# Performance work log

Measured on AMD Instinct MI355X. Metric: run time of the kernel, lower is better.

Reference implementation:

```python
import jax, jax.numpy as jnp
import numpy as np

B, F, H, L, K = 16384, 1024, 1024, 256, 7

def _lin(key, fi, fo, lead=()):
    k1, k2 = jax.random.split(key)
    s = 1.0 / np.sqrt(fi)
    W = jax.random.uniform(k1, lead + (fi, fo), jnp.float32, -s, s)
    b = jax.random.uniform(k2, lead + (fo,), jnp.float32, -s, s)
    return W, b

def setup_inputs() -> dict:
    ks = jax.random.split(jax.random.key(0), 16)
    x = jax.random.normal(ks[0], (B, F), jnp.float32)
    t = jax.random.randint(ks[1], (B,), 0, K, jnp.int32)
    y = jax.random.normal(ks[2], (B,), jnp.float32)
    d = jax.random.normal(ks[3], (B,), jnp.float32)
    tw0, tb0 = _lin(ks[4], F, L)
    tw1, tb1 = _lin(ks[5], L, L)
    tw2, tb2 = _lin(ks[6], L, K)
    yw0, yb0 = _lin(ks[7], F, H)
    yw1, yb1 = _lin(ks[8], H, H)
    yhW, yhb = _lin(ks[9], H, 2, (K,))
    dw0, db0 = _lin(ks[10], F, H)
    dw1, db1 = _lin(ks[11], H, H)
    dhW, dhb = _lin(ks[12], H, 2, (K,))
    zw0, zb0 = _lin(ks[13], F + 2, H)
    zw1, zb1 = _lin(ks[14], H, H)
    zhW, zhb = _lin(ks[15], H, 2 * L, (K,))
    return dict(x=x, t=t, y=y, d=d, tw0=tw0, tb0=tb0, tw1=tw1, tb1=tb1, tw2=tw2, tb2=tb2,
                yw0=yw0, yb0=yb0, yw1=yw1, yb1=yb1, yhW=yhW, yhb=yhb,
                dw0=dw0, db0=db0, dw1=dw1, db1=db1, dhW=dhW, dhb=dhb,
                zw0=zw0, zb0=zb0, zw1=zw1, zb1=zb1, zhW=zhW, zhb=zhb)

def _mlp2(x, w0, b0, w1, b1):
    # FullyConnected([in, H, H], final_activation=ELU)
    return jax.nn.elu(jax.nn.elu(x @ w0 + b0) @ w1 + b1)

def _select(hidden, t, hW, hb):
    # dense compute of all K treatment heads, then per-row gather by t
    all_out = jnp.einsum('bh,khd->bkd', hidden, hW) + hb  # [B, K, D]
    return jnp.take_along_axis(all_out, t[:, None, None], axis=1)[:, 0]

def _normal_head(sel):
    # pyro NormalNet head on a scalar outcome
    loc = jnp.clip(sel[:, 0:1], -1e6, 1e6)
    scale = jnp.minimum(jax.nn.softplus(sel[:, 1:2]) + 1e-3, 1e6)
    return loc, scale

def _diagnormal_head(sel):
    loc = jnp.clip(sel[:, :L], -100.0, 100.0)
    scale = jnp.minimum(jax.nn.softplus(sel[:, L:]) + 0.001, 100.0)
    return loc, scale

def reference(x, t, y, d, tw0, tb0, tw1, tb1, tw2, tb2,
              yw0, yb0, yw1, yb1, yhW, yhb,
              dw0, db0, dw1, db1, dhW, dhb,
              zw0, zb0, zw1, zb1, zhW, zhb):
    # t_nn: MultinormNet, ELU final activation then clamp(-10, 10)
    t_logits = jnp.clip(jax.nn.elu(_mlp2(x, tw0, tb0, tw1, tb1) @ tw2 + tb2), -10.0, 10.0)
    # y_dist(t, x)
    hy = _mlp2(x, yw0, yb0, yw1, yb1)
    y_loc, y_scale = _normal_head(_select(hy, t, yhW, yhb))
    # d_dist(t, x)
    hd = _mlp2(x, dw0, db0, dw1, db1)
    d_loc, d_scale = _normal_head(_select(hd, t, dhW, dhb))
    # z_dist(y, d, t, x): hidden from cat([y, d, x])
    hz = _mlp2(jnp.concatenate([y[:, None], d[:, None], x], axis=-1), zw0, zb0, zw1, zb1)
    z_loc, z_scale = _diagnormal_head(_select(hz, t, zhW, zhb))
    # [B, K + 4 + 2L]
    return jnp.concatenate([t_logits, y_loc, y_scale, d_loc, d_scale, z_loc, z_scale], axis=-1)
```

## Files before the change

kernel.cpp:

```cpp
#include <hip/hip_runtime.h>
#include <hip/hip_bf16.h>
#include <cstdint>
#include <cstddef>

typedef __hip_bfloat16 bf16;
typedef __bf16 bf16x8 __attribute__((ext_vector_type(8)));
typedef float f32x4 __attribute__((ext_vector_type(4)));

#define DEVFN static __device__ __forceinline__

DEVFN void async16(const void* g, void* l) {
  __builtin_amdgcn_global_load_lds(
      (const __attribute__((address_space(1))) uint32_t*)g,
      (__attribute__((address_space(3))) uint32_t*)l, 16, 0, 0);
}

DEVFN float eluf(float v) { return v > 0.f ? v : expm1f(v); }
DEVFN float softplusf(float x) {
  return x > 0.f ? x + log1pf(expf(-x)) : log1pf(expf(x));
}

template <int NAH, int NBH, int NFB>
DEVFN void kloop32(const bf16* (&gA)[NAH], const bf16* (&gB)[NBH], bf16* As,
                   bf16* Bs, int tid, const bf16* aBase, const bf16* bBase,
                   int colsel, f32x4 (&acc)[4][NFB], int kiters) {
  for (int kt = 0; kt < kiters; ++kt) {
#pragma unroll
    for (int c = 0; c < NAH; ++c) async16(gA[c], As + c * 2048 + tid * 8);
#pragma unroll
    for (int c = 0; c < NBH; ++c) async16(gB[c], Bs + c * 2048 + tid * 8);
#pragma unroll
    for (int c = 0; c < NAH; ++c) gA[c] += 32;
#pragma unroll
    for (int c = 0; c < NBH; ++c) gB[c] += 32;
    __syncthreads();
    bf16x8 af[4], bfv[NFB];
#pragma unroll
    for (int r = 0; r < 4; ++r) af[r] = *(const bf16x8*)(aBase + r * 512 + colsel);
#pragma unroll
    for (int c = 0; c < NFB; ++c) bfv[c] = *(const bf16x8*)(bBase + c * 512 + colsel);
#pragma unroll
    for (int r = 0; r < 4; ++r)
#pragma unroll
      for (int c = 0; c < NFB; ++c)
        acc[r][c] = __builtin_amdgcn_mfma_f32_16x16x32_bf16(af[r], bfv[c], acc[r][c], 0, 0, 0);
    __syncthreads();
  }
}

DEVFN int swz_scol(int tid) { return (((tid & 3) ^ ((tid >> 3) & 3)) * 8); }
DEVFN int swz_colsel(int quad, int l15) { return ((quad ^ ((l15 >> 1) & 3)) * 8); }

DEVFN void transpose_tile(const float* src, bf16* dst, int R, int C, int bx, int by) {
  __shared__ float tile[32][33];
  const int c0 = bx * 32, r0 = by * 32;
  const int tx = threadIdx.x & 31, ty = threadIdx.x >> 5;
#pragma unroll
  for (int rr = ty; rr < 32; rr += 8)
    tile[rr][tx] = src[(size_t)(r0 + rr) * C + c0 + tx];
  __syncthreads();
#pragma unroll
  for (int rr = ty; rr < 32; rr += 8)
    dst[(size_t)(c0 + rr) * R + r0 + tx] = __float2bfloat16(tile[tx][rr]);
}

__global__ __launch_bounds__(256) void prep_all_k(
    const float* __restrict__ x, bf16* __restrict__ xb,
    const float* __restrict__ yw0, const float* __restrict__ dw0,
    const float* __restrict__ zw0, const float* __restrict__ tw0,
    bf16* __restrict__ BtL1,
    const float* __restrict__ yw1, const float* __restrict__ dw1,
    const float* __restrict__ zw1, bf16* __restrict__ BtL2,
    const float* __restrict__ tw1, bf16* __restrict__ tw1t,
    const float* __restrict__ zhW, bf16* __restrict__ zhWt,
    const float* __restrict__ yb0, const float* __restrict__ db0,
    const float* __restrict__ zb0, const float* __restrict__ tb0,
    const float* __restrict__ yb1, const float* __restrict__ db1,
    const float* __restrict__ zb1,
    float* __restrict__ biasAll, float* __restrict__ r0All,
    float* __restrict__ r1All, float* __restrict__ biasL2,
    const int* __restrict__ t, int* __restrict__ cnt, int* __restrict__ seg,
    int* __restrict__ rank, int* __restrict__ sids) {
  int l = blockIdx.x;
  if (l < 8192) {
    size_t i = ((size_t)l * 256 + threadIdx.x) * 8;
    float4 v0 = *(const float4*)(x + i);
    float4 v1 = *(const float4*)(x + i + 4);
    union { bf16 h[8]; uint4 u; } o;
    o.h[0] = __float2bfloat16(v0.x); o.h[1] = __float2bfloat16(v0.y);
    o.h[2] = __float2bfloat16(v0.z); o.h[3] = __float2bfloat16(v0.w);
    o.h[4] = __float2bfloat16(v1.x); o.h[5] = __float2bfloat16(v1.y);
    o.h[6] = __float2bfloat16(v1.z); o.h[7] = __float2bfloat16(v1.w);
    *(uint4*)(xb + i) = o.u;
    return;
  }
  l -= 8192;
  if (l < 4096) {
    int z = l >> 10, rem = l & 1023, bx = rem & 31, by = rem >> 5;
    const float* src = (z == 0) ? yw0 : (z == 1) ? dw0 : (z == 2) ? zw0 + 2048 : tw0;
    int C = (z == 3) ? 256 : 1024;
    if (bx * 32 < C)
      transpose_tile(src, BtL1 + (size_t)z * 1024 * 1024, 1024, C, bx, by);
    return;
  }
  l -= 4096;
  if (l < 3072) {
    int z = l >> 10, rem = l & 1023, bx = rem & 31, by = rem >> 5;
    const float* src = (z == 0) ? yw1 : (z == 1) ? dw1 : zw1;
    transpose_tile(src, BtL2 + (size_t)z * 1024 * 1024, 1024, 1024, bx, by);
    return;
  }
  l -= 3072;
  if (l < 64) {
    transpose_tile(tw1, tw1t, 256, 256, l & 7, l >> 3);
    return;
  }
  l -= 64;
  if (l < 3584) {
    int z = l >> 9, rem = l & 511, bx = rem & 15, by = rem >> 4;
    transpose_tile(zhW + (size_t)z * 1024 * 512, zhWt + (size_t)z * 512 * 1024,
                   1024, 512, bx, by);
    return;
  }
  l -= 3584;
  if (l < 13) {
    int i = l * 256 + threadIdx.x;
    if (i >= 3328) return;
    float b;
    if (i < 1024) b = yb0[i];
    else if (i < 2048) b = db0[i - 1024];
    else if (i < 3072) b = zb0[i - 2048];
    else b = tb0[i - 3072];
    biasAll[i] = b;
    bool inz = (i >= 2048 && i < 3072);
    r0All[i] = inz ? zw0[i - 2048] : 0.f;
    r1All[i] = inz ? zw0[1024 + (i - 2048)] : 0.f;
    if (i < 3072)
      biasL2[i] = (i < 1024) ? yb1[i] : (i < 2048) ? db1[i - 1024] : zb1[i - 2048];
    return;
  }
  {
    __shared__ int h[8], sseg[8];
    const int tid = threadIdx.x;
    if (tid < 8) h[tid] = 0;
    __syncthreads();
    const int base = tid * 64;
    int lc[7] = {0, 0, 0, 0, 0, 0, 0};
    for (int i = 0; i < 64; ++i) lc[t[base + i]]++;
    int myoff[7];
#pragma unroll
    for (int k = 0; k < 7; ++k) myoff[k] = atomicAdd(&h[k], lc[k]);
    __syncthreads();
    if (tid == 0) {
      int s = 0;
      for (int k = 0; k < 7; ++k) { sseg[k] = s; s += h[k]; }
      sseg[7] = s;
    }
    __syncthreads();
    if (tid < 7) { cnt[tid] = h[tid]; seg[tid] = sseg[tid]; }
    if (tid == 7) seg[7] = sseg[7];
    int cur[7];
#pragma unroll
    for (int k = 0; k < 7; ++k) cur[k] = sseg[k] + myoff[k];
    for (int i = 0; i < 64; ++i) {
      int b = base + i, k = t[b];
      int r = cur[k]++;
      rank[b] = r;
      sids[r] = b;
    }
  }
}

__global__ __launch_bounds__(256) void gemm_l1_k(
    const bf16* __restrict__ A, const bf16* __restrict__ Bt,
    const float* __restrict__ biasAll, const float* __restrict__ r0All,
    const float* __restrict__ r1All, const float* __restrict__ yv,
    const float* __restrict__ dv, bf16* __restrict__ a1y,
    bf16* __restrict__ a1d, bf16* __restrict__ a1z, bf16* __restrict__ ht1) {
  __shared__ bf16 As[128 * 32];
  __shared__ bf16 Bs[128 * 32];
  const int tid = threadIdx.x, lane = tid & 63, wid = tid >> 6;
  const int wm = wid >> 1, wn = wid & 1, quad = lane >> 4, l15 = lane & 15;
  const int id = blockIdx.x;
  const int xcd = id & 7, lid = id >> 3;
  const int pass = lid / 208, rem = lid - pass * 208;
  const int mt = xcd * 16 + pass * 8 + (rem & 7), nt = rem >> 3;
  const int bm0 = mt * 128, bn0 = nt * 128;
  const int sr = tid >> 2, scol = swz_scol(tid);
  const bf16* gA[2];
  const bf16* gB[2];
#pragma unroll
  for (int c = 0; c < 2; ++c) {
    gA[c] = A + (size_t)(bm0 + c * 64 + sr) * 1024 + scol;
    gB[c] = Bt + (size_t)(bn0 + c * 64 + sr) * 1024 + scol;
  }
  const bf16* aBase = &As[(wm * 64 + l15) * 32];
  const bf16* bBase = &Bs[(wn * 64 + l15) * 32];
  const int colsel = swz_colsel(quad, l15);
  f32x4 acc[4][4] = {};
  kloop32<2, 2, 4>(gA, gB, As, Bs, tid, aBase, bBase, colsel, acc, 32);

  const int g = nt >> 3;
  bf16* dst = (g == 0) ? a1y : (g == 1) ? a1d : (g == 2) ? a1z : ht1;
  const int ldc = (g == 3) ? 256 : 1024;
  const int colb = bn0 - g * 1024;
  float bv[4], z0[4], z1[4];
#pragma unroll
  for (int c = 0; c < 4; ++c) {
    int gn = bn0 + wn * 64 + c * 16 + l15;
    bv[c] = biasAll[gn]; z0[c] = r0All[gn]; z1[c] = r1All[gn];
  }
#pragma unroll
  for (int r = 0; r < 4; ++r) {
#pragma unroll
    for (int q = 0; q < 4; ++q) {
      int gm = bm0 + wm * 64 + r * 16 + quad * 4 + q;
      float yy = yv[gm], dd = dv[gm];
#pragma unroll
      for (int c = 0; c < 4; ++c) {
        float v = acc[r][c][q] + bv[c] + yy * z0[c] + dd * z1[c];
        dst[(size_t)gm * ldc + colb + wn * 64 + c * 16 + l15] = __float2bfloat16(eluf(v));
      }
    }
  }
}

__global__ __launch_bounds__(256) void gemm_l2t_k(
    const bf16* __restrict__ a1y, const bf16* __restrict__ a1d,
    const bf16* __restrict__ a1z, const bf16* __restrict__ ht1,
    const bf16* __restrict__ BtL2, const bf16* __restrict__ tw1t,
    const float* __restrict__ biasL2, const float* __restrict__ tb1,
    bf16* __restrict__ hyd, bf16* __restrict__ hzg, bf16* __restrict__ ht2,
    const int* __restrict__ rank) {
  __shared__ bf16 As[128 * 32];
  __shared__ bf16 Bs[128 * 32];
  const int tid = threadIdx.x, lane = tid & 63, wid = tid >> 6;
  const int wm = wid >> 1, wn = wid & 1, quad = lane >> 4, l15 = lane & 15;
  const int id = blockIdx.x;
  int bm0, bn0, Ka, g;
  const bf16 *Aptr, *Bptr;
  if (id < 3072) {
    const int xcd = id & 7, lid = id >> 3;
    const int pass = lid / 192, rem = lid - pass * 192;
    const int mt = xcd * 16 + pass * 8 + (rem & 7), nt = rem >> 3;
    bm0 = mt * 128; bn0 = nt * 128; Ka = 1024;
    g = nt >> 3;
    Aptr = (g == 0) ? a1y : (g == 1) ? a1d : a1z;
    Bptr = BtL2;
  } else {
    const int local = id - 3072;
    bm0 = (local >> 1) * 128; bn0 = (local & 1) * 128; Ka = 256;
    g = 3; Aptr = ht1; Bptr = tw1t;
  }
  const int sr = tid >> 2, scol = swz_scol(tid);
  const bf16* gA[2];
  const bf16* gB[2];
#pragma unroll
  for (int c = 0; c < 2; ++c) {
    gA[c] = Aptr + (size_t)(bm0 + c * 64 + sr) * Ka + scol;
    gB[c] = Bptr + (size_t)(bn0 + c * 64 + sr) * Ka + scol;
  }
  const bf16* aBase = &As[(wm * 64 + l15) * 32];
  const bf16* bBase = &Bs[(wn * 64 + l15) * 32];
  const int colsel = swz_colsel(quad, l15);
  f32x4 acc[4][4] = {};
  kloop32<2, 2, 4>(gA, gB, As, Bs, tid, aBase, bBase, colsel, acc, Ka >> 5);

  const float* bias = (g == 3) ? tb1 : biasL2;
  float bv[4];
#pragma unroll
  for (int c = 0; c < 4; ++c) bv[c] = bias[bn0 + wn * 64 + c * 16 + l15];
#pragma unroll
  for (int r = 0; r < 4; ++r) {
#pragma unroll
    for (int q = 0; q < 4; ++q) {
      int gm = bm0 + wm * 64 + r * 16 + quad * 4 + q;
      bf16* dst; size_t rowoff;
      if (g == 2) { dst = hzg; rowoff = (size_t)rank[gm] * 1024 + (size_t)(bn0 - 2048); }
      else if (g == 3) { dst = ht2; rowoff = (size_t)gm * 256 + bn0; }
      else { dst = hyd; rowoff = (size_t)gm * 2048 + bn0; }
#pragma unroll
      for (int c = 0; c < 4; ++c) {
        float v = acc[r][c][q] + bv[c];
        dst[rowoff + wn * 64 + c * 16 + l15] = __float2bfloat16(eluf(v));
      }
    }
  }
}

#define ZMT 28
#define ZB (7 * ZMT * 8)
__global__ __launch_bounds__(256) void tail_k(
    const bf16* __restrict__ hzg, const bf16* __restrict__ zhWt,
    const float* __restrict__ zhb, const int* __restrict__ seg,
    const int* __restrict__ cnts, const int* __restrict__ sids,
    const bf16* __restrict__ hyd, const bf16* __restrict__ ht2,
    const int* __restrict__ t, const float* __restrict__ yhW,
    const float* __restrict__ yhb, const float* __restrict__ dhW,
    const float* __restrict__ dhb, const float* __restrict__ tw2,
    const float* __restrict__ tb2, float* __restrict__ out) {
  __shared__ bf16 As[128 * 32];
  __shared__ bf16 Bs[64 * 32];
  const int tid = threadIdx.x, lane = tid & 63, wid = tid >> 6;
  const int wv = wid, quad = lane >> 4, l15 = lane & 15;
  if (blockIdx.x < ZB) {
    const int kb = blockIdx.x / (ZMT * 8);
    const int r = blockIdx.x % (ZMT * 8);
    const int cnt = cnts[kb];
    const int bm0 = (r >> 3) * 128;
    if (bm0 >= cnt) return;
    const int n0 = (r & 7) * 64;
    const int wm = wid >> 1, wn = wid & 1;
    const int base = seg[kb];
    const int sr = tid >> 2, scol = swz_scol(tid);
    const bf16* gA[2];
    const bf16* gB[1];
#pragma unroll
    for (int c = 0; c < 2; ++c) {
      int rr = bm0 + c * 64 + sr;
      if (rr >= cnt) rr = cnt - 1;
      gA[c] = hzg + (size_t)(base + rr) * 1024 + scol;
    }
    gB[0] = zhWt + (size_t)kb * 512 * 1024 + (size_t)(n0 + sr) * 1024 + scol;
    const bf16* aBase = &As[(wm * 64 + l15) * 32];
    const bf16* bBase = &Bs[(wn * 32 + l15) * 32];
    const int colsel = swz_colsel(quad, l15);
    f32x4 acc[4][2] = {};
    kloop32<2, 1, 2>(gA, gB, As, Bs, tid, aBase, bBase, colsel, acc, 32);
    const float* bias = zhb + (size_t)kb * 512;
    float bv[2]; int gnn[2];
#pragma unroll
    for (int c = 0; c < 2; ++c) {
      gnn[c] = n0 + wn * 32 + c * 16 + l15;
      bv[c] = bias[gnn[c]];
    }
#pragma unroll
    for (int r2 = 0; r2 < 4; ++r2)
#pragma unroll
      for (int q = 0; q < 4; ++q) {
        int lm = bm0 + wm * 64 + r2 * 16 + quad * 4 + q;
        if (lm < cnt) {
          int gm = sids[base + lm];
          size_t ob = (size_t)gm * 523 + 11;
#pragma unroll
          for (int c = 0; c < 2; ++c) {
            float v = acc[r2][c][q] + bv[c];
            int n = gnn[c];
            out[ob + n] = (n < 256) ? fminf(fmaxf(v, -100.f), 100.f)
                                    : fminf(softplusf(v) + 0.001f, 100.f);
          }
        }
      }
    return;
  }
  const int hid = blockIdx.x - ZB;
  if (hid < 4096) {
    const int b = hid * 4 + wv;
    const int tb = t[b];
    const float* yW = yhW + (size_t)tb * 2048;
    const float* dW = dhW + (size_t)tb * 2048;
    float s0 = 0.f, s1 = 0.f, s2 = 0.f, s3 = 0.f;
    for (int i = lane; i < 1024; i += 64) {
      float a = __bfloat162float(hyd[(size_t)b * 2048 + i]);
      float c = __bfloat162float(hyd[(size_t)b * 2048 + 1024 + i]);
      s0 += a * yW[2 * i]; s1 += a * yW[2 * i + 1];
      s2 += c * dW[2 * i]; s3 += c * dW[2 * i + 1];
    }
#pragma unroll
    for (int off = 32; off > 0; off >>= 1) {
      s0 += __shfl_down(s0, off); s1 += __shfl_down(s1, off);
      s2 += __shfl_down(s2, off); s3 += __shfl_down(s3, off);
    }
    if (lane == 0) {
      size_t o = (size_t)b * 523;
      out[o + 7] = fminf(fmaxf(s0 + yhb[tb * 2], -1e6f), 1e6f);
      out[o + 8] = fminf(softplusf(s1 + yhb[tb * 2 + 1]) + 1e-3f, 1e6f);
      out[o + 9] = fminf(fmaxf(s2 + dhb[tb * 2], -1e6f), 1e6f);
      out[o + 10] = fminf(softplusf(s3 + dhb[tb * 2 + 1]) + 1e-3f, 1e6f);
    }
  } else {
    const int b = (hid - 4096) * 4 + wv;
    float h[4];
#pragma unroll
    for (int j = 0; j < 4; ++j)
      h[j] = __bfloat162float(ht2[(size_t)b * 256 + lane * 4 + j]);
    float pp[7];
#pragma unroll
    for (int kk = 0; kk < 7; ++kk) {
      float s = 0.f;
#pragma unroll
      for (int j = 0; j < 4; ++j) s += h[j] * tw2[(lane * 4 + j) * 7 + kk];
      pp[kk] = s;
    }
#pragma unroll
    for (int kk = 0; kk < 7; ++kk)
#pragma unroll
      for (int off = 32; off > 0; off >>= 1) pp[kk] += __shfl_down(pp[kk], off);
    if (lane == 0) {
#pragma unroll
      for (int kk = 0; kk < 7; ++kk) {
        float v = eluf(pp[kk] + tb2[kk]);
        out[(size_t)b * 523 + kk] = fminf(fmaxf(v, -10.f), 10.f);
      }
    }
  }
}

extern "C" void kernel_launch(void* const* d_in, const int* in_sizes, int n_in,
                              void* d_out, int out_size, void* d_ws, size_t ws_size,
                              hipStream_t stream) {
  const float* x   = (const float*)d_in[0];
  const int*   t   = (const int*)d_in[1];
  const float* yv  = (const float*)d_in[2];
  const float* dv  = (const float*)d_in[3];
  const float* tw0 = (const float*)d_in[4];
  const float* tb0 = (const float*)d_in[5];
  const float* tw1 = (const float*)d_in[6];
  const float* tb1 = (const float*)d_in[7];
  const float* tw2 = (const float*)d_in[8];
  const float* tb2 = (const float*)d_in[9];
  const float* yw0 = (const float*)d_in[10];
  const float* yb0 = (const float*)d_in[11];
  const float* yw1 = (const float*)d_in[12];
  const float* yb1 = (const float*)d_in[13];
  const float* yhW = (const float*)d_in[14];
  const float* yhb = (const float*)d_in[15];
  const float* dw0 = (const float*)d_in[16];
  const float* db0 = (const float*)d_in[17];
  const float* dw1 = (const float*)d_in[18];
  const float* db1 = (const float*)d_in[19];
  const float* dhW = (const float*)d_in[20];
  const float* dhb = (const float*)d_in[21];
  const float* zw0 = (const float*)d_in[22];
  const float* zb0 = (const float*)d_in[23];
  const float* zw1 = (const float*)d_in[24];
  const float* zb1 = (const float*)d_in[25];
  const float* zhW = (const float*)d_in[26];
  const float* zhb = (const float*)d_in[27];
  float* out = (float*)d_out;

  const int B = 16384;
  char* p = (char*)d_ws;
  auto take = [&](size_t bytes) {
    char* r = p;
    p += (bytes + 255) & ~(size_t)255;
    return r;
  };
  bf16*  BtL1    = (bf16*)take((size_t)3328 * 1024 * 2);
  bf16*  BtL2    = (bf16*)take((size_t)3072 * 1024 * 2);
  bf16*  tw1t    = (bf16*)take((size_t)256 * 256 * 2);
  bf16*  zhWt    = (bf16*)take((size_t)7 * 512 * 1024 * 2);
  float* biasAll = (float*)take(3328 * 4);
  float* r0All   = (float*)take(3328 * 4);
  float* r1All   = (float*)take(3328 * 4);
  float* biasL2  = (float*)take(3072 * 4);
  int*   cnt     = (int*)take(8 * 4);
  int*   seg     = (int*)take(8 * 4);
  int*   rank    = (int*)take((size_t)B * 4);
  int*   sids    = (int*)take((size_t)B * 4);
  bf16*  xb      = (bf16*)take((size_t)B * 1024 * 2);
  bf16*  a1y     = (bf16*)take((size_t)B * 1024 * 2);
  bf16*  a1d     = (bf16*)take((size_t)B * 1024 * 2);
  bf16*  a1z     = (bf16*)take((size_t)B * 1024 * 2);
  bf16*  ht1     = (bf16*)take((size_t)B * 256 * 2);
  bf16*  hyd     = (bf16*)take((size_t)B * 2048 * 2);
  bf16*  ht2     = (bf16*)take((size_t)B * 256 * 2);
  bf16*  hzg     = xb;

  prep_all_k<<<19022, 256, 0, stream>>>(x, xb, yw0, dw0, zw0, tw0, BtL1,
                                        yw1, dw1, zw1, BtL2, tw1, tw1t, zhW, zhWt,
                                        yb0, db0, zb0, tb0, yb1, db1, zb1,
                                        biasAll, r0All, r1All, biasL2,
                                        t, cnt, seg, rank, sids);
  gemm_l1_k<<<3328, 256, 0, stream>>>(xb, BtL1, biasAll, r0All, r1All,
                                      yv, dv, a1y, a1d, a1z, ht1);
  gemm_l2t_k<<<3328, 256, 0, stream>>>(a1y, a1d, a1z, ht1, BtL2, tw1t,
                                       biasL2, tb1, hyd, hzg, ht2, rank);
  tail_k<<<ZB + 8192, 256, 0, stream>>>(hzg, zhWt, zhb, seg, cnt, sids,
                                        hyd, ht2, t, yhW, yhb, dhW, dhb,
                                        tw2, tb2, out);
}
```

Before: 680.0 us.

## Switch layer GEMMs to 256x256 tiles with double-buffered 8-wave pipeline

The two large GEMM kernels move from 128x128 tiles with 4 waves and a single-buffered 32-wide K loop to 256x256 tiles with 8 waves and 64-wide K steps. The K loop is double-buffered in 128 KB of LDS and interleaves async global-to-LDS loads with MFMA phases, using raw s_barrier/s_waitcnt and setprio. The goals are more data reuse per loaded byte, fewer blocks, and hiding load latency behind compute. In exchange the large LDS footprint limits occupancy, the hand-written waitcnt and barrier scheduling is fragile, and the tail tiles for the t-net become coarser.

```diff
diff --git a/kernel.cpp b/kernel.cpp
--- a/kernel.cpp
+++ b/kernel.cpp
@@ -8,6 +8,8 @@
 typedef float f32x4 __attribute__((ext_vector_type(4)));
 
 #define DEVFN static __device__ __forceinline__
+#define BAR() asm volatile("s_barrier" ::: "memory")
+#define VMCNT(n) asm volatile("s_waitcnt vmcnt(" #n ")" ::: "memory")
 
 DEVFN void async16(const void* g, void* l) {
   __builtin_amdgcn_global_load_lds(
@@ -18,6 +20,116 @@
 DEVFN float eluf(float v) { return v > 0.f ? v : expm1f(v); }
 DEVFN float softplusf(float x) {
   return x > 0.f ? x + log1pf(expf(-x)) : log1pf(expf(x));
+}
+
+
+DEVFN void stage_half(const bf16* p, int ld, bf16* reg, int tid) {
+  async16(p, reg + tid * 8);
+  async16(p + (size_t)64 * ld, reg + 4096 + tid * 8);
+}
+
+template <int PART>
+DEVFN void stage_ht(const bf16* pA, const bf16* pB, int lda, int ldb,
+                    bf16* lds, int tid, int t) {
+  bf16* base = lds + (t & 1) * 32768;
+  if constexpr (PART == 0)
+    stage_half(pA + (size_t)t * 64, lda, base, tid);
+  else if constexpr (PART == 1)
+    stage_half(pA + (size_t)t * 64 + (size_t)128 * lda, lda, base + 8192, tid);
+  else if constexpr (PART == 2)
+    stage_half(pB + (size_t)t * 64, ldb, base + 16384, tid);
+  else
+    stage_half(pB + (size_t)t * 64 + (size_t)128 * ldb, ldb, base + 24576, tid);
+}
+
+template <int MB, int NB>
+DEVFN void mfma8(f32x4 (&acc)[8][4], const bf16x8 (&af)[8][2],
+                 const bf16x8 (&bv)[2][2]) {
+#pragma unroll
+  for (int mf = 0; mf < 4; ++mf)
+#pragma unroll
+    for (int nf = 0; nf < 2; ++nf) {
+      acc[MB + mf][NB + nf] = __builtin_amdgcn_mfma_f32_16x16x32_bf16(
+          af[MB + mf][0], bv[nf][0], acc[MB + mf][NB + nf], 0, 0, 0);
+      acc[MB + mf][NB + nf] = __builtin_amdgcn_mfma_f32_16x16x32_bf16(
+          af[MB + mf][1], bv[nf][1], acc[MB + mf][NB + nf], 0, 0, 0);
+    }
+}
+
+DEVFN void quad_phases(const bf16* Ab, const bf16* Bb, int cs0, int cs1,
+                       f32x4 (&acc)[8][4], const bf16* pA, const bf16* pB,
+                       int lda, int ldb, bf16* lds, int tid,
+                       int tB1, int tN, bool st0, bool stN, int vmend) {
+  bf16x8 af[8][2], b0[2][2], b1[2][2];
+#pragma unroll
+  for (int mf = 0; mf < 8; ++mf) {
+    af[mf][0] = *(const bf16x8*)(Ab + mf * 1024 + cs0);
+    af[mf][1] = *(const bf16x8*)(Ab + mf * 1024 + cs1);
+  }
+#pragma unroll
+  for (int nf = 0; nf < 2; ++nf) {
+    b0[nf][0] = *(const bf16x8*)(Bb + nf * 1024 + cs0);
+    b0[nf][1] = *(const bf16x8*)(Bb + nf * 1024 + cs1);
+  }
+  if (st0) stage_ht<3>(pA, pB, lda, ldb, lds, tid, tB1);
+  BAR();
+  __builtin_amdgcn_s_setprio(1);
+  mfma8<0, 0>(acc, af, b0);
+  __builtin_amdgcn_s_setprio(0);
+  BAR();
+#pragma unroll
+  for (int nf = 0; nf < 2; ++nf) {
+    b1[nf][0] = *(const bf16x8*)(Bb + (2 + nf) * 1024 + cs0);
+    b1[nf][1] = *(const bf16x8*)(Bb + (2 + nf) * 1024 + cs1);
+  }
+  if (stN) stage_ht<0>(pA, pB, lda, ldb, lds, tid, tN);
+  BAR();
+  __builtin_amdgcn_s_setprio(1);
+  mfma8<0, 2>(acc, af, b1);
+  __builtin_amdgcn_s_setprio(0);
+  BAR();
+  if (stN) stage_ht<1>(pA, pB, lda, ldb, lds, tid, tN);
+  BAR();
+  __builtin_amdgcn_s_setprio(1);
+  mfma8<4, 0>(acc, af, b0);
+  __builtin_amdgcn_s_setprio(0);
+  BAR();
+  if (stN) stage_ht<2>(pA, pB, lda, ldb, lds, tid, tN);
+  BAR();
+  __builtin_amdgcn_s_setprio(1);
+  mfma8<4, 2>(acc, af, b1);
+  __builtin_amdgcn_s_setprio(0);
+  if (vmend == 0) { VMCNT(0); }
+  else if (vmend > 0) { VMCNT(6); }
+  BAR();
+}
+
+DEVFN void gemm256(const bf16* pA, const bf16* pB, int lda, int ldb, int NT,
+                   bf16* lds, int tid, int wm, int wn, int quad, int l15,
+                   f32x4 (&acc)[8][4]) {
+  const int k7 = l15 & 7;
+  const int cs0 = (quad ^ k7) * 8;
+  const int cs1 = ((quad + 4) ^ k7) * 8;
+  const bf16* Abase = lds + wm * 8192 + l15 * 64;
+  const bf16* Bbase = lds + 16384 + (wn >> 1) * 8192 + ((wn & 1) * 64 + l15) * 64;
+  stage_ht<0>(pA, pB, lda, ldb, lds, tid, 0);
+  stage_ht<1>(pA, pB, lda, ldb, lds, tid, 0);
+  stage_ht<2>(pA, pB, lda, ldb, lds, tid, 0);
+  stage_ht<3>(pA, pB, lda, ldb, lds, tid, 0);
+  stage_ht<0>(pA, pB, lda, ldb, lds, tid, 1);
+  stage_ht<1>(pA, pB, lda, ldb, lds, tid, 1);
+  stage_ht<2>(pA, pB, lda, ldb, lds, tid, 1);
+  VMCNT(6);
+  BAR();
+  const int NI = NT >> 1;
+  for (int j = 0; j < NI; ++j) {
+    const bool last = (j == NI - 1);
+    const int a = 2 * j;
+    quad_phases(Abase, Bbase, cs0, cs1, acc, pA, pB, lda, ldb, lds, tid,
+                a + 1, a + 2, true, !last, last ? 0 : 6);
+    quad_phases(Abase + 32768, Bbase + 32768, cs0, cs1, acc, pA, pB, lda, ldb,
+                lds, tid, a + 2, a + 3, !last, !last, last ? -1 : 6);
+  }
 }
 
 template <int NAH, int NBH, int NFB>
@@ -171,118 +283,101 @@
   }
 }
 
-__global__ __launch_bounds__(256) void gemm_l1_k(
+__global__ __launch_bounds__(512, 2) void gemm_l1_k(
     const bf16* __restrict__ A, const bf16* __restrict__ Bt,
     const float* __restrict__ biasAll, const float* __restrict__ r0All,
     const float* __restrict__ r1All, const float* __restrict__ yv,
     const float* __restrict__ dv, bf16* __restrict__ a1y,
     bf16* __restrict__ a1d, bf16* __restrict__ a1z, bf16* __restrict__ ht1) {
-  __shared__ bf16 As[128 * 32];
-  __shared__ bf16 Bs[128 * 32];
+  __shared__ bf16 lds[65536];
   const int tid = threadIdx.x, lane = tid & 63, wid = tid >> 6;
-  const int wm = wid >> 1, wn = wid & 1, quad = lane >> 4, l15 = lane & 15;
+  const int wm = wid >> 2, wn = wid & 3, quad = lane >> 4, l15 = lane & 15;
   const int id = blockIdx.x;
   const int xcd = id & 7, lid = id >> 3;
-  const int pass = lid / 208, rem = lid - pass * 208;
-  const int mt = xcd * 16 + pass * 8 + (rem & 7), nt = rem >> 3;
-  const int bm0 = mt * 128, bn0 = nt * 128;
-  const int sr = tid >> 2, scol = swz_scol(tid);
-  const bf16* gA[2];
-  const bf16* gB[2];
-#pragma unroll
-  for (int c = 0; c < 2; ++c) {
-    gA[c] = A + (size_t)(bm0 + c * 64 + sr) * 1024 + scol;
-    gB[c] = Bt + (size_t)(bn0 + c * 64 + sr) * 1024 + scol;
-  }
-  const bf16* aBase = &As[(wm * 64 + l15) * 32];
-  const bf16* bBase = &Bs[(wn * 64 + l15) * 32];
-  const int colsel = swz_colsel(quad, l15);
-  f32x4 acc[4][4] = {};
-  kloop32<2, 2, 4>(gA, gB, As, Bs, tid, aBase, bBase, colsel, acc, 32);
-
-  const int g = nt >> 3;
+  const int mt = xcd * 8 + (lid & 7), nt = lid >> 3;
+  const int bm0 = mt * 256, bn0 = nt * 256;
+  const int srow = tid >> 3, scol = ((tid & 7) ^ ((tid >> 3) & 7)) * 8;
+  const bf16* pA = A + (size_t)(bm0 + srow) * 1024 + scol;
+  const bf16* pB = Bt + (size_t)(bn0 + srow) * 1024 + scol;
+  f32x4 acc[8][4] = {};
+  gemm256(pA, pB, 1024, 1024, 16, lds, tid, wm, wn, quad, l15, acc);
+
+  const int g = nt >> 2;
   bf16* dst = (g == 0) ? a1y : (g == 1) ? a1d : (g == 2) ? a1z : ht1;
   const int ldc = (g == 3) ? 256 : 1024;
   const int colb = bn0 - g * 1024;
   float bv[4], z0[4], z1[4];
 #pragma unroll
-  for (int c = 0; c < 4; ++c) {
-    int gn = bn0 + wn * 64 + c * 16 + l15;
-    bv[c] = biasAll[gn]; z0[c] = r0All[gn]; z1[c] = r1All[gn];
-  }
-#pragma unroll
-  for (int r = 0; r < 4; ++r) {
+  for (int nf = 0; nf < 4; ++nf) {
+    int gn = bn0 + wn * 64 + nf * 16 + l15;
+    bv[nf] = biasAll[gn]; z0[nf] = r0All[gn]; z1[nf] = r1All[gn];
+  }
+#pragma unroll
+  for (int mf = 0; mf < 8; ++mf) {
+    const int rbase = bm0 + wm * 128 + mf * 16 + quad * 4;
+    const float4 y4 = *(const float4*)(yv + rbase);
+    const float4 d4 = *(const float4*)(dv + rbase);
 #pragma unroll
     for (int q = 0; q < 4; ++q) {
-      int gm = bm0 + wm * 64 + r * 16 + quad * 4 + q;
-      float yy = yv[gm], dd = dv[gm];
-#pragma unroll
-      for (int c = 0; c < 4; ++c) {
-        float v = acc[r][c][q] + bv[c] + yy * z0[c] + dd * z1[c];
-        dst[(size_t)gm * ldc + colb + wn * 64 + c * 16 + l15] = __float2bfloat16(eluf(v));
+      const float yy = (&y4.x)[q], dd = (&d4.x)[q];
+      const size_t ro = (size_t)(rbase + q) * ldc + colb + wn * 64;
+#pragma unroll
+      for (int nf = 0; nf < 4; ++nf) {
+        float v = acc[mf][nf][q] + bv[nf] + yy * z0[nf] + dd * z1[nf];
+        dst[ro + nf * 16 + l15] = __float2bfloat16(eluf(v));
       }
     }
   }
 }
 
-__global__ __launch_bounds__(256) void gemm_l2t_k(
+__global__ __launch_bounds__(512, 2) void gemm_l2t_k(
     const bf16* __restrict__ a1y, const bf16* __restrict__ a1d,
     const bf16* __restrict__ a1z, const bf16* __restrict__ ht1,
     const bf16* __restrict__ BtL2, const bf16* __restrict__ tw1t,
     const float* __restrict__ biasL2, const float* __restrict__ tb1,
     bf16* __restrict__ hyd, bf16* __restrict__ hzg, bf16* __restrict__ ht2,
     const int* __restrict__ rank) {
-  __shared__ bf16 As[128 * 32];
-  __shared__ bf16 Bs[128 * 32];
+  __shared__ bf16 lds[65536];
   const int tid = threadIdx.x, lane = tid & 63, wid = tid >> 6;
-  const int wm = wid >> 1, wn = wid & 1, quad = lane >> 4, l15 = lane & 15;
+  const int wm = wid >> 2, wn = wid & 3, quad = lane >> 4, l15 = lane & 15;
   const int id = blockIdx.x;
   int bm0, bn0, Ka, g;
   const bf16 *Aptr, *Bptr;
-  if (id < 3072) {
+  if (id < 768) {
     const int xcd = id & 7, lid = id >> 3;
-    const int pass = lid / 192, rem = lid - pass * 192;
-    const int mt = xcd * 16 + pass * 8 + (rem & 7), nt = rem >> 3;
-    bm0 = mt * 128; bn0 = nt * 128; Ka = 1024;
-    g = nt >> 3;
+    const int mt = xcd * 8 + (lid & 7), nt = lid >> 3;
+    bm0 = mt * 256; bn0 = nt * 256; Ka = 1024;
+    g = nt >> 2;
     Aptr = (g == 0) ? a1y : (g == 1) ? a1d : a1z;
     Bptr = BtL2;
   } else {
-    const int local = id - 3072;
-    bm0 = (local >> 1) * 128; bn0 = (local & 1) * 128; Ka = 256;
+    const int local = id - 768;
+    bm0 = local * 256; bn0 = 0; Ka = 256;
     g = 3; Aptr = ht1; Bptr = tw1t;
   }
-  const int sr = tid >> 2, scol = swz_scol(tid);
-  const bf16* gA[2];
-  const bf16* gB[2];
-#pragma unroll
-  for (int c = 0; c < 2; ++c) {
-    gA[c] = Aptr + (size_t)(bm0 + c * 64 + sr) * Ka + scol;
-    gB[c] = Bptr + (size_t)(bn0 + c * 64 + sr) * Ka + scol;
-  }
-  const bf16* aBase = &As[(wm * 64 + l15) * 32];
-  const bf16* bBase = &Bs[(wn * 64 + l15) * 32];
-  const int colsel = swz_colsel(quad, l15);
-  f32x4 acc[4][4] = {};
-  kloop32<2, 2, 4>(gA, gB, As, Bs, tid, aBase, bBase, colsel, acc, Ka >> 5);
+  const int srow = tid >> 3, scol = ((tid & 7) ^ ((tid >> 3) & 7)) * 8;
+  const bf16* pA = Aptr + (size_t)(bm0 + srow) * Ka + scol;
+  const bf16* pB = Bptr + (size_t)(bn0 + srow) * Ka + scol;
+  f32x4 acc[8][4] = {};
+  gemm256(pA, pB, Ka, Ka, Ka >> 6, lds, tid, wm, wn, quad, l15, acc);
 
   const float* bias = (g == 3) ? tb1 : biasL2;
   float bv[4];
 #pragma unroll
-  for (int c = 0; c < 4; ++c) bv[c] = bias[bn0 + wn * 64 + c * 16 + l15];
-#pragma unroll
-  for (int r = 0; r < 4; ++r) {
+  for (int nf = 0; nf < 4; ++nf) bv[nf] = bias[bn0 + wn * 64 + nf * 16 + l15];
+#pragma unroll
+  for (int mf = 0; mf < 8; ++mf) {
 #pragma unroll
     for (int q = 0; q < 4; ++q) {
-      int gm = bm0 + wm * 64 + r * 16 + quad * 4 + q;
+      const int gm = bm0 + wm * 128 + mf * 16 + quad * 4 + q;
       bf16* dst; size_t rowoff;
       if (g == 2) { dst = hzg; rowoff = (size_t)rank[gm] * 1024 + (size_t)(bn0 - 2048); }
-      else if (g == 3) { dst = ht2; rowoff = (size_t)gm * 256 + bn0; }
+      else if (g == 3) { dst = ht2; rowoff = (size_t)gm * 256; }
       else { dst = hyd; rowoff = (size_t)gm * 2048 + bn0; }
 #pragma unroll
-      for (int c = 0; c < 4; ++c) {
-        float v = acc[r][c][q] + bv[c];
-        dst[rowoff + wn * 64 + c * 16 + l15] = __float2bfloat16(eluf(v));
+      for (int nf = 0; nf < 4; ++nf) {
+        float v = acc[mf][nf][q] + bv[nf];
+        dst[rowoff + wn * 64 + nf * 16 + l15] = __float2bfloat16(eluf(v));
       }
     }
   }
@@ -472,10 +567,10 @@
                                         yb0, db0, zb0, tb0, yb1, db1, zb1,
                                         biasAll, r0All, r1All, biasL2,
                                         t, cnt, seg, rank, sids);
-  gemm_l1_k<<<3328, 256, 0, stream>>>(xb, BtL1, biasAll, r0All, r1All,
-                                      yv, dv, a1y, a1d, a1z, ht1);
-  gemm_l2t_k<<<3328, 256, 0, stream>>>(a1y, a1d, a1z, ht1, BtL2, tw1t,
-                                       biasL2, tb1, hyd, hzg, ht2, rank);
+  gemm_l1_k<<<832, 512, 0, stream>>>(xb, BtL1, biasAll, r0All, r1All,
+                                     yv, dv, a1y, a1d, a1z, ht1);
+  gemm_l2t_k<<<832, 512, 0, stream>>>(a1y, a1d, a1z, ht1, BtL2, tw1t,
+                                      biasL2, tb1, hyd, hzg, ht2, rank);
   tail_k<<<ZB + 8192, 256, 0, stream>>>(hzg, zhWt, zhb, seg, cnt, sids,
                                         hyd, ht2, t, yhW, yhb, dhW, dhb,
                                         tw2, tb2, out);
```

Result: slower. 919.1 us (+35.2%).

## Rewrite layer GEMMs with 256x256 tiles, 32x32 MFMA and pipelined LDS staging

Applied to the files above, without the earlier changes.

Replaces the 128x128 tile GEMM loop in both layer kernels with a 256x256 tile per 512-thread block. It uses the 32x32x16 bf16 MFMA, a double-buffered 64-deep K stage with async global-to-LDS loads, and hand-placed waitcnt/barrier interleaving to overlap loads with MFMA. The aim is more operand reuse and less global/LDS traffic per FLOP, and hiding memory latency. In exchange, occupancy drops to one block per CU with 128KB LDS, and there are fewer blocks, which risks tail imbalance and correctness bugs from the manual synchronisation.

```diff
diff --git a/kernel.cpp b/kernel.cpp
--- a/kernel.cpp
+++ b/kernel.cpp
@@ -6,8 +6,13 @@
 typedef __hip_bfloat16 bf16;
 typedef __bf16 bf16x8 __attribute__((ext_vector_type(8)));
 typedef float f32x4 __attribute__((ext_vector_type(4)));
+typedef float f32x16 __attribute__((ext_vector_type(16)));
 
 #define DEVFN static __device__ __forceinline__
+#define SBAR() __builtin_amdgcn_s_barrier()
+#define SCHED0() __builtin_amdgcn_sched_barrier(0)
+#define VMCNT(n) asm volatile("s_waitcnt vmcnt(" #n ")")
+#define LGKM(n) asm volatile("s_waitcnt lgkmcnt(" #n ")")
 
 DEVFN void async16(const void* g, void* l) {
   __builtin_amdgcn_global_load_lds(
@@ -15,9 +20,107 @@
       (__attribute__((address_space(3))) uint32_t*)l, 16, 0, 0);
 }
 
+DEVFN bf16x8 dsr(const bf16* p) {
+  bf16x8 r;
+  asm volatile("ds_read_b128 %0, %1"
+               : "=v"(r)
+               : "v"((const __attribute__((address_space(3))) bf16*)p));
+  return r;
+}
+
 DEVFN float eluf(float v) { return v > 0.f ? v : expm1f(v); }
 DEVFN float softplusf(float x) {
   return x > 0.f ? x + log1pf(expf(-x)) : log1pf(expf(x));
+}
+
+
+struct FragSet {
+  bf16x8 a[4];
+  bf16x8 b[2];
+};
+
+DEVFN void gemm256(const bf16* __restrict__ pA, const bf16* __restrict__ pB,
+                   int lda, int ldb, int NT, bf16* lds, int tid, int wm, int wn,
+                   int hi, int l31, f32x16 (&acc)[4][2]) {
+  const int k2 = l31 & 3;
+  const int swe = (hi ^ k2) * 8;
+  const int swo = ((2 + hi) ^ k2) * 8;
+  const int rowA = (wm * 128 + l31) * 32;
+  const int rowB = (wn * 64 + l31) * 32;
+
+  auto READ = [&](FragSet& f, int t, int kk) {
+    const bf16* base = lds + (t & 1) * 32768 + (kk >> 1) * 8192 +
+                       ((kk & 1) ? swo : swe);
+    const bf16* A = base + rowA;
+    const bf16* B = base + 16384 + rowB;
+#pragma unroll
+    for (int mf = 0; mf < 4; ++mf) f.a[mf] = dsr(A + mf * 1024);
+#pragma unroll
+    for (int nf = 0; nf < 2; ++nf) f.b[nf] = dsr(B + nf * 1024);
+  };
+  auto STAGE = [&](int t, int reg) {
+    bf16* dst = lds + (t & 1) * 32768 + ((reg >> 1) ? 16384 : 0) +
+                (reg & 1) * 8192 + tid * 8;
+    const bf16* src =
+        ((reg >> 1) ? pB : pA) + (size_t)t * 64 + (reg & 1) * 32;
+    const int ld = (reg >> 1) ? ldb : lda;
+    async16(src, dst);
+    async16(src + (size_t)128 * ld, dst + 4096);
+  };
+  auto MF = [&](const FragSet& f) {
+    __builtin_amdgcn_s_setprio(1);
+#pragma unroll
+    for (int mf = 0; mf < 4; ++mf)
+#pragma unroll
+      for (int nf = 0; nf < 2; ++nf)
+        acc[mf][nf] = __builtin_amdgcn_mfma_f32_32x32x16_bf16(
+            f.a[mf], f.b[nf], acc[mf][nf], 0, 0, 0);
+    __builtin_amdgcn_s_setprio(0);
+  };
+
+  FragSet fA, fB;
+  STAGE(0, 0); STAGE(0, 2); STAGE(0, 1); STAGE(0, 3);
+  STAGE(1, 0);
+  VMCNT(6);
+  SBAR();
+  SCHED0();
+  READ(fA, 0, 0);
+
+  for (int t = 0; t < NT; ++t) {
+    const bool n1 = (t + 1 < NT), n2 = (t + 2 < NT);
+    READ(fB, t, 1);
+    LGKM(6);
+    if (n1) STAGE(t + 1, 2);
+    SBAR(); SCHED0();
+    MF(fA);
+    VMCNT(4);
+    SBAR(); SCHED0();
+    READ(fA, t, 2);
+    LGKM(6);
+    if (n1) STAGE(t + 1, 1);
+    SBAR(); SCHED0();
+    MF(fB);
+    VMCNT(4);
+    SBAR(); SCHED0();
+    READ(fB, t, 3);
+    LGKM(6);
+    if (n1) STAGE(t + 1, 3);
+    SBAR(); SCHED0();
+    MF(fA);
+    VMCNT(4);
+    SBAR(); SCHED0();
+    if (n1) {
+      READ(fA, t + 1, 0);
+      LGKM(6);
+    } else {
+      LGKM(0);
+    }
+    if (n2) STAGE(t + 2, 0);
+    SBAR(); SCHED0();
+    MF(fB);
+    if (n1) { VMCNT(4); }
+    SBAR(); SCHED0();
+  }
 }
 
 template <int NAH, int NBH, int NFB>
@@ -171,118 +274,108 @@
   }
 }
 
-__global__ __launch_bounds__(256) void gemm_l1_k(
+__global__ __launch_bounds__(512, 1) void gemm_l1_k(
     const bf16* __restrict__ A, const bf16* __restrict__ Bt,
     const float* __restrict__ biasAll, const float* __restrict__ r0All,
     const float* __restrict__ r1All, const float* __restrict__ yv,
     const float* __restrict__ dv, bf16* __restrict__ a1y,
     bf16* __restrict__ a1d, bf16* __restrict__ a1z, bf16* __restrict__ ht1) {
-  __shared__ bf16 As[128 * 32];
-  __shared__ bf16 Bs[128 * 32];
+  __shared__ bf16 lds[65536];
   const int tid = threadIdx.x, lane = tid & 63, wid = tid >> 6;
-  const int wm = wid >> 1, wn = wid & 1, quad = lane >> 4, l15 = lane & 15;
+  const int wm = wid >> 2, wn = wid & 3, hi = lane >> 5, l31 = lane & 31;
   const int id = blockIdx.x;
   const int xcd = id & 7, lid = id >> 3;
-  const int pass = lid / 208, rem = lid - pass * 208;
-  const int mt = xcd * 16 + pass * 8 + (rem & 7), nt = rem >> 3;
-  const int bm0 = mt * 128, bn0 = nt * 128;
-  const int sr = tid >> 2, scol = swz_scol(tid);
-  const bf16* gA[2];
-  const bf16* gB[2];
-#pragma unroll
-  for (int c = 0; c < 2; ++c) {
-    gA[c] = A + (size_t)(bm0 + c * 64 + sr) * 1024 + scol;
-    gB[c] = Bt + (size_t)(bn0 + c * 64 + sr) * 1024 + scol;
-  }
-  const bf16* aBase = &As[(wm * 64 + l15) * 32];
-  const bf16* bBase = &Bs[(wn * 64 + l15) * 32];
-  const int colsel = swz_colsel(quad, l15);
-  f32x4 acc[4][4] = {};
-  kloop32<2, 2, 4>(gA, gB, As, Bs, tid, aBase, bBase, colsel, acc, 32);
-
-  const int g = nt >> 3;
+  const int mt = xcd * 8 + (lid & 7), nt = lid >> 3;
+  const int bm0 = mt * 256, bn0 = nt * 256;
+  const int srow = tid >> 2, sg = (((tid & 3) ^ ((tid >> 2) & 3)) * 8);
+  const bf16* pA = A + (size_t)(bm0 + srow) * 1024 + sg;
+  const bf16* pB = Bt + (size_t)(bn0 + srow) * 1024 + sg;
+  f32x16 acc[4][2] = {};
+  gemm256(pA, pB, 1024, 1024, 16, lds, tid, wm, wn, hi, l31, acc);
+
+  const int g = nt >> 2;
   bf16* dst = (g == 0) ? a1y : (g == 1) ? a1d : (g == 2) ? a1z : ht1;
   const int ldc = (g == 3) ? 256 : 1024;
   const int colb = bn0 - g * 1024;
-  float bv[4], z0[4], z1[4];
-#pragma unroll
-  for (int c = 0; c < 4; ++c) {
-    int gn = bn0 + wn * 64 + c * 16 + l15;
-    bv[c] = biasAll[gn]; z0[c] = r0All[gn]; z1[c] = r1All[gn];
-  }
-#pragma unroll
-  for (int r = 0; r < 4; ++r) {
-#pragma unroll
-    for (int q = 0; q < 4; ++q) {
-      int gm = bm0 + wm * 64 + r * 16 + quad * 4 + q;
-      float yy = yv[gm], dd = dv[gm];
-#pragma unroll
-      for (int c = 0; c < 4; ++c) {
-        float v = acc[r][c][q] + bv[c] + yy * z0[c] + dd * z1[c];
-        dst[(size_t)gm * ldc + colb + wn * 64 + c * 16 + l15] = __float2bfloat16(eluf(v));
+  float bvv[2], z0v[2], z1v[2];
+#pragma unroll
+  for (int nf = 0; nf < 2; ++nf) {
+    int gn = bn0 + wn * 64 + nf * 32 + l31;
+    bvv[nf] = biasAll[gn]; z0v[nf] = r0All[gn]; z1v[nf] = r1All[gn];
+  }
+#pragma unroll
+  for (int mf = 0; mf < 4; ++mf) {
+#pragma unroll
+    for (int rg = 0; rg < 4; ++rg) {
+      const int r0 = bm0 + wm * 128 + mf * 32 + rg * 8 + hi * 4;
+      const float4 y4 = *(const float4*)(yv + r0);
+      const float4 d4 = *(const float4*)(dv + r0);
+#pragma unroll
+      for (int q = 0; q < 4; ++q) {
+        const float yy = (&y4.x)[q], dd = (&d4.x)[q];
+        const size_t ro = (size_t)(r0 + q) * ldc + colb + wn * 64;
+#pragma unroll
+        for (int nf = 0; nf < 2; ++nf) {
+          float v = acc[mf][nf][rg * 4 + q] + bvv[nf] + yy * z0v[nf] + dd * z1v[nf];
+          dst[ro + nf * 32 + l31] = __float2bfloat16(eluf(v));
+        }
       }
     }
   }
 }
 
-__global__ __launch_bounds__(256) void gemm_l2t_k(
+__global__ __launch_bounds__(512, 1) void gemm_l2t_k(
     const bf16* __restrict__ a1y, const bf16* __restrict__ a1d,
     const bf16* __restrict__ a1z, const bf16* __restrict__ ht1,
     const bf16* __restrict__ BtL2, const bf16* __restrict__ tw1t,
     const float* __restrict__ biasL2, const float* __restrict__ tb1,
     bf16* __restrict__ hyd, bf16* __restrict__ hzg, bf16* __restrict__ ht2,
     const int* __restrict__ rank) {
-  __shared__ bf16 As[128 * 32];
-  __shared__ bf16 Bs[128 * 32];
+  __shared__ bf16 lds[65536];
   const int tid = threadIdx.x, lane = tid & 63, wid = tid >> 6;
-  const int wm = wid >> 1, wn = wid & 1, quad = lane >> 4, l15 = lane & 15;
+  const int wm = wid >> 2, wn = wid & 3, hi = lane >> 5, l31 = lane & 31;
   const int id = blockIdx.x;
   int bm0, bn0, Ka, g;
   const bf16 *Aptr, *Bptr;
-  if (id < 3072) {
+  if (id < 768) {
     const int xcd = id & 7, lid = id >> 3;
-    const int pass = lid / 192, rem = lid - pass * 192;
-    const int mt = xcd * 16 + pass * 8 + (rem & 7), nt = rem >> 3;
-    bm0 = mt * 128; bn0 = nt * 128; Ka = 1024;
-    g = nt >> 3;
+    const int mt = xcd * 8 + (lid & 7), nt = lid >> 3;
+    bm0 = mt * 256; bn0 = nt * 256; Ka = 1024;
+    g = nt >> 2;
     Aptr = (g == 0) ? a1y : (g == 1) ? a1d : a1z;
     Bptr = BtL2;
   } else {
-    const int local = id - 3072;
-    bm0 = (local >> 1) * 128; bn0 = (local & 1) * 128; Ka = 256;
+    const int local = id - 768;
+    bm0 = local * 256; bn0 = 0; Ka = 256;
     g = 3; Aptr = ht1; Bptr = tw1t;
   }
-  const int sr = tid >> 2, scol = swz_scol(tid);
-  const bf16* gA[2];
-  const bf16* gB[2];
-#pragma unroll
-  for (int c = 0; c < 2; ++c) {
-    gA[c] = Aptr + (size_t)(bm0 + c * 64 + sr) * Ka + scol;
-    gB[c] = Bptr + (size_t)(bn0 + c * 64 + sr) * Ka + scol;
-  }
-  const bf16* aBase = &As[(wm * 64 + l15) * 32];
-  const bf16* bBase = &Bs[(wn * 64 + l15) * 32];
-  const int colsel = swz_colsel(quad, l15);
-  f32x4 acc[4][4] = {};
-  kloop32<2, 2, 4>(gA, gB, As, Bs, tid, aBase, bBase, colsel, acc, Ka >> 5);
+  const int srow = tid >> 2, sg = (((tid & 3) ^ ((tid >> 2) & 3)) * 8);
+  const bf16* pA = Aptr + (size_t)(bm0 + srow) * Ka + sg;
+  const bf16* pB = Bptr + (size_t)(bn0 + srow) * Ka + sg;
+  f32x16 acc[4][2] = {};
+  gemm256(pA, pB, Ka, Ka, Ka >> 6, lds, tid, wm, wn, hi, l31, acc);
 
   const float* bias = (g == 3) ? tb1 : biasL2;
-  float bv[4];
-#pragma unroll
-  for (int c = 0; c < 4; ++c) bv[c] = bias[bn0 + wn * 64 + c * 16 + l15];
-#pragma unroll
-  for (int r = 0; r < 4; ++r) {
-#pragma unroll
-    for (int q = 0; q < 4; ++q) {
-      int gm = bm0 + wm * 64 + r * 16 + quad * 4 + q;
-      bf16* dst; size_t rowoff;
-      if (g == 2) { dst = hzg; rowoff = (size_t)rank[gm] * 1024 + (size_t)(bn0 - 2048); }
-      else if (g == 3) { dst = ht2; rowoff = (size_t)gm * 256 + bn0; }
-      else { dst = hyd; rowoff = (size_t)gm * 2048 + bn0; }
-#pragma unroll
-      for (int c = 0; c < 4; ++c) {
-        float v = acc[r][c][q] + bv[c];
-        dst[rowoff + wn * 64 + c * 16 + l15] = __float2bfloat16(eluf(v));
+  float bvv[2];
+#pragma unroll
+  for (int nf = 0; nf < 2; ++nf) bvv[nf] = bias[bn0 + wn * 64 + nf * 32 + l31];
+#pragma unroll
+  for (int mf = 0; mf < 4; ++mf) {
+#pragma unroll
+    for (int rg = 0; rg < 4; ++rg) {
+      const int r0 = bm0 + wm * 128 + mf * 32 + rg * 8 + hi * 4;
+#pragma unroll
+      for (int q = 0; q < 4; ++q) {
+        const int gm = r0 + q;
+        bf16* dst; size_t rowoff;
+        if (g == 2) { dst = hzg; rowoff = (size_t)rank[gm] * 1024 + (size_t)(bn0 - 2048); }
+        else if (g == 3) { dst = ht2; rowoff = (size_t)gm * 256; }
+        else { dst = hyd; rowoff = (size_t)gm * 2048 + bn0; }
+#pragma unroll
+        for (int nf = 0; nf < 2; ++nf) {
+          float v = acc[mf][nf][rg * 4 + q] + bvv[nf];
+          dst[rowoff + wn * 64 + nf * 32 + l31] = __float2bfloat16(eluf(v));
+        }
       }
     }
   }
@@ -472,10 +565,10 @@
                                         yb0, db0, zb0, tb0, yb1, db1, zb1,
                                         biasAll, r0All, r1All, biasL2,
                                         t, cnt, seg, rank, sids);
-  gemm_l1_k<<<3328, 256, 0, stream>>>(xb, BtL1, biasAll, r0All, r1All,
-                                      yv, dv, a1y, a1d, a1z, ht1);
-  gemm_l2t_k<<<3328, 256, 0, stream>>>(a1y, a1d, a1z, ht1, BtL2, tw1t,
-                                       biasL2, tb1, hyd, hzg, ht2, rank);
+  gemm_l1_k<<<832, 512, 0, stream>>>(xb, BtL1, biasAll, r0All, r1All,
+                                     yv, dv, a1y, a1d, a1z, ht1);
+  gemm_l2t_k<<<832, 512, 0, stream>>>(a1y, a1d, a1z, ht1, BtL2, tw1t,
+                                      biasL2, tb1, hyd, hzg, ht2, rank);
   tail_k<<<ZB + 8192, 256, 0, stream>>>(hzg, zhWt, zhb, seg, cnt, sids,
                                         hyd, ht2, t, yhW, yhb, dhW, dhb,
                                         tw2, tb2, out);
```

Measured after the change: 740.9 us. 9.0% more time.
